# Optimization experiments

Hardware: AMD Instinct MI355X
Metric: run time of the kernel (lower is better)

## Reference

```python
import jax, jax.numpy as jnp
import numpy as np

H = 4          # heads
C = 32         # out_channels per head
NEG_SLOPE = 0.2
N_NODES = 50000
N_EDGES = 600000
F_IN = 128
OUT_DIM = 10
N_GRAPHS = 32


def _gat_params(keys, f_in, scale=0.05):
    hc = H * C
    return dict(
        Wl=jax.random.normal(keys[0], (f_in, hc)) * scale,
        bl=jnp.zeros((hc,)),
        Wr=jax.random.normal(keys[1], (f_in, hc)) * scale,
        br=jnp.zeros((hc,)),
        We=jax.random.normal(keys[2], (1, hc)) * scale,   # lin_edge, bias=False in PyG
        att=jax.random.normal(keys[3], (H, C)) * scale,
        bias=jnp.zeros((hc,)),
    )


def setup_inputs() -> dict:
    key = jax.random.key(0)
    ks = jax.random.split(key, 16)
    x = jax.random.normal(ks[0], (N_NODES, F_IN), dtype=jnp.float32)
    edge_index = jax.random.randint(ks[1], (2, N_EDGES), 0, N_NODES, dtype=jnp.int32)
    edge_weight = jax.random.uniform(ks[2], (N_EDGES, 1), dtype=jnp.float32)
    batch = jnp.sort(jax.random.randint(ks[3], (N_NODES,), 0, N_GRAPHS, dtype=jnp.int32))
    p1 = _gat_params(ks[4:8], F_IN)
    p2 = _gat_params(ks[8:12], H * C)
    fc_W = jax.random.normal(ks[12], (H * C, OUT_DIM)) * 0.05
    fc_b = jnp.zeros((OUT_DIM,))
    return dict(
        x=x, edge_index=edge_index, edge_weight=edge_weight, batch=batch,
        p1_Wl=p1['Wl'], p1_bl=p1['bl'], p1_Wr=p1['Wr'], p1_br=p1['br'],
        p1_We=p1['We'], p1_att=p1['att'], p1_bias=p1['bias'],
        p2_Wl=p2['Wl'], p2_bl=p2['bl'], p2_Wr=p2['Wr'], p2_br=p2['br'],
        p2_We=p2['We'], p2_att=p2['att'], p2_bias=p2['bias'],
        fc_W=fc_W, fc_b=fc_b,
    )


def _add_self_loops(src, dst, eattr, n):
    # PyG fill_value='mean': self-loop attr = mean of incoming edge_attr per node
    loop = jnp.arange(n, dtype=src.dtype)
    cnt = jax.ops.segment_sum(jnp.ones((src.shape[0],), eattr.dtype), dst, num_segments=n)
    loop_attr = jax.ops.segment_sum(eattr, dst, num_segments=n) / jnp.maximum(cnt, 1.0)[:, None]
    return (jnp.concatenate([src, loop]), jnp.concatenate([dst, loop]),
            jnp.concatenate([eattr, loop_attr], axis=0))


def _gatv2_conv(x, src, dst, eattr, Wl, bl, Wr, br, We, att, bias, n):
    x_l = (x @ Wl + bl).reshape(n, H, C)   # source transform
    x_r = (x @ Wr + br).reshape(n, H, C)   # target transform
    e_feat = (eattr @ We).reshape(-1, H, C)
    # per-edge message [E2, H, C]
    m = jax.nn.leaky_relu(x_l[src] + x_r[dst] + e_feat, NEG_SLOPE)
    alpha = jnp.einsum('ehc,hc->eh', m, att)            # [E2, H]
    amax = jax.ops.segment_max(alpha, dst, num_segments=n)
    amax = jnp.where(jnp.isfinite(amax), amax, 0.0)
    ex = jnp.exp(alpha - amax[dst])
    denom = jax.ops.segment_sum(ex, dst, num_segments=n)
    a = ex / (denom[dst] + 1e-16)                       # segment softmax
    out = jax.ops.segment_sum(a[:, :, None] * x_l[src], dst, num_segments=n)
    return out.reshape(n, H * C) + bias


def reference(x, edge_index, edge_weight, batch,
              p1_Wl, p1_bl, p1_Wr, p1_br, p1_We, p1_att, p1_bias,
              p2_Wl, p2_bl, p2_Wr, p2_br, p2_We, p2_att, p2_bias,
              fc_W, fc_b):
    n = x.shape[0]
    src, dst, eattr = _add_self_loops(edge_index[0], edge_index[1], edge_weight, n)
    h = _gatv2_conv(x, src, dst, eattr, p1_Wl, p1_bl, p1_Wr, p1_br, p1_We, p1_att, p1_bias, n)
    h = _gatv2_conv(h, src, dst, eattr, p2_Wl, p2_bl, p2_Wr, p2_br, p2_We, p2_att, p2_bias, n)
    cnt = jax.ops.segment_sum(jnp.ones((n,), h.dtype), batch, num_segments=N_GRAPHS)
    pooled = jax.ops.segment_sum(h, batch, num_segments=N_GRAPHS) / jnp.maximum(cnt, 1.0)[:, None]
    out = pooled @ fc_W + fc_b
    return out, pooled
```

## Files before the change

### kernel.cpp

```cpp
#include <hip/hip_runtime.h>
#include <hip/hip_bf16.h>
#include <cstdint>

static inline int cdiv(int a, int b){ return (a + b - 1) / b; }

typedef __attribute__((ext_vector_type(8))) short short8v;
typedef __attribute__((ext_vector_type(4))) float float4v;

#define ELLW 48

__device__ inline float bf2f(unsigned short u){ return __uint_as_float(((unsigned)u) << 16); }
__device__ inline unsigned short f2bf(float f){
  unsigned u = __float_as_uint(f);
  u += 0x7fffu + ((u >> 16) & 1u);
  return (unsigned short)(u >> 16);
}
__device__ inline float4 ldbf4(const unsigned short* p){
  ushort4 u = *(const ushort4*)p;
  return make_float4(bf2f(u.x), bf2f(u.y), bf2f(u.z), bf2f(u.w));
}
__device__ inline int sniff16(const unsigned* __restrict__ xw){
  int good = 0;
  #pragma unroll
  for (int j = 0; j < 16; ++j){
    float v = __uint_as_float(xw[j] << 16);
    float a = fabsf(v);
    good += (v == 0.f) || (a >= 6.1e-5f && a <= 64.f);
  }
  return good > 8;
}

struct P16 { const void* p[16]; };
__global__ void k_prep(P16 s, const unsigned* __restrict__ xw,
                       unsigned long long* __restrict__ deg64, float* __restrict__ pool,
                       int pz, int N,
                       unsigned short* __restrict__ Wf, unsigned short* __restrict__ bb,
                       unsigned short* __restrict__ sm){
  int i = blockIdx.x * blockDim.x + threadIdx.x;
  if (i < N) deg64[i] = 0ull;
  if (i < pz) pool[i] = 0.f;
  if (i >= 68106) return;
  const int bf = sniff16(xw);
  auto rd = [&](const void* q, int j) -> unsigned short {
    return bf ? ((const unsigned short*)q)[j] : f2bf(((const float*)q)[j]);
  };
  if (i < 65536){
    int l = i >> 15, r = i & 32767;
    int j = r & 7, n = (r >> 3) & 255, kq = r >> 11;
    int k = kq * 8 + j;
    const void* W = (n < 128) ? (l ? s.p[7] : s.p[0]) : (l ? s.p[9] : s.p[2]);
    Wf[i] = rd(W, k * 128 + (n & 127));
  } else if (i < 66048){
    int i2 = i - 65536;
    int l = i2 >> 8, n = i2 & 255;
    const void* b = (n < 128) ? (l ? s.p[8] : s.p[1]) : (l ? s.p[10] : s.p[3]);
    bb[i2] = rd(b, n & 127);
  } else {
    int j = i - 66048;
    const void* q; int o;
    if      (j < 128){ q = s.p[4];  o = j; }
    else if (j < 256){ q = s.p[5];  o = j - 128; }
    else if (j < 384){ q = s.p[6];  o = j - 256; }
    else if (j < 512){ q = s.p[11]; o = j - 384; }
    else if (j < 640){ q = s.p[12]; o = j - 512; }
    else if (j < 768){ q = s.p[13]; o = j - 640; }
    else if (j < 2048){ q = s.p[14]; o = j - 768; }
    else { q = s.p[15]; o = j - 2048; }
    sm[j] = rd(q, o);
  }
}

__global__ __launch_bounds__(256)
void k_esc(const int* __restrict__ ei, const void* __restrict__ ew,
           const unsigned* __restrict__ xw,
           unsigned long long* __restrict__ deg64, unsigned* __restrict__ eE,
           int E, int P, int N){
  const int bf = sniff16(xw);
  const int part = blockIdx.x & 7;
  const int lo = part * P;
  const int hi = min(lo + P, N);
  const int base = (int)(blockIdx.x >> 3) * 2048;
  const int end = min(base + 2048, E);
  for (int e = base + (int)threadIdx.x; e < end; e += 256){
    int dst = ei[E + e];
    if (dst < lo || dst >= hi) continue;
    int src = ei[e];
    unsigned short w16; float w;
    if (bf){ w16 = ((const unsigned short*)ew)[e]; w = bf2f(w16); }
    else   { w = ((const float*)ew)[e]; w16 = f2bf(w); }
    unsigned long long pk = (1ull << 40) + (unsigned long long)(unsigned)(w * 1048576.0f + 0.5f);
    unsigned long long old = atomicAdd(&deg64[dst], pk);
    int pos = min((int)(old >> 40), ELLW - 1);
    eE[dst * ELLW + pos] = (unsigned)src | ((unsigned)w16 << 16);
  }
}

template<bool ACT_BF_FIXED>
__global__ __launch_bounds__(256)
void k_gemm2(const void* __restrict__ actv, const unsigned* __restrict__ xw,
             const unsigned short* __restrict__ Wf, const unsigned short* __restrict__ bb,
             unsigned short* __restrict__ outL, unsigned short* __restrict__ outR, int nrows){
  __shared__ unsigned short As[64][136];
  const int abf = ACT_BF_FIXED ? 1 : sniff16(xw);
  const int t = threadIdx.x;
  const int row0 = blockIdx.x * 64;
  for (int c = t; c < 2048; c += 256){
    int row = c >> 5, col4 = (c & 31) * 4;
    int r = row0 + row;
    ushort4 v = make_ushort4(0, 0, 0, 0);
    if (r < nrows){
      if (abf) v = *(const ushort4*)((const unsigned short*)actv + (size_t)r * 128 + col4);
      else {
        float4 f = *(const float4*)((const float*)actv + (size_t)r * 128 + col4);
        v.x = f2bf(f.x); v.y = f2bf(f.y); v.z = f2bf(f.z); v.w = f2bf(f.w);
      }
    }
    *(ushort4*)&As[row][col4] = v;
  }
  __syncthreads();
  const int wv = t >> 6, lane = t & 63;
  const int l15 = lane & 15, q = lane >> 4;
  #pragma unroll
  for (int half = 0; half < 2; ++half){
    const int ntb = wv * 4 + half * 2;
    short8v bfr[2][4];
    #pragma unroll
    for (int nt = 0; nt < 2; ++nt){
      int n = (ntb + nt) * 16 + l15;
      #pragma unroll
      for (int ks = 0; ks < 4; ++ks)
        bfr[nt][ks] = *(const short8v*)(Wf + ((((ks * 4 + q) * 256 + n)) << 3));
    }
    float4v acc[4][2];
    #pragma unroll
    for (int mi = 0; mi < 4; ++mi)
      #pragma unroll
      for (int nt = 0; nt < 2; ++nt)
        acc[mi][nt] = (float4v){0.f, 0.f, 0.f, 0.f};
    #pragma unroll
    for (int mi = 0; mi < 4; ++mi){
      short8v afr[4];
      #pragma unroll
      for (int ks = 0; ks < 4; ++ks)
        afr[ks] = *(const short8v*)&As[mi * 16 + l15][ks * 32 + q * 8];
      #pragma unroll
      for (int nt = 0; nt < 2; ++nt)
        #pragma unroll
        for (int ks = 0; ks < 4; ++ks)
          acc[mi][nt] = __builtin_amdgcn_mfma_f32_16x16x32_bf16(afr[ks], bfr[nt][ks], acc[mi][nt], 0, 0, 0);
    }
    #pragma unroll
    for (int nt = 0; nt < 2; ++nt){
      int n = (ntb + nt) * 16 + l15;
      float bias = bf2f(bb[n]);
      unsigned short* outp = (n < 128) ? outL : outR;
      int nc = n & 127;
      #pragma unroll
      for (int mi = 0; mi < 4; ++mi)
        #pragma unroll
        for (int rr = 0; rr < 4; ++rr){
          int grow = row0 + mi * 16 + q * 4 + rr;
          if (grow < nrows) outp[(size_t)grow * 128 + nc] = f2bf(acc[mi][nt][rr] + bias);
        }
    }
  }
}

__global__ __launch_bounds__(256)
void k_node(const unsigned short* __restrict__ A, const unsigned short* __restrict__ B,
            const unsigned long long* __restrict__ deg64, const unsigned* __restrict__ eE,
            const unsigned short* __restrict__ We, const unsigned short* __restrict__ att,
            const unsigned short* __restrict__ bias, unsigned short* __restrict__ H, int N){
  int node = (blockIdx.x * 256 + threadIdx.x) >> 5;
  if (node >= N) return;
  int lane = threadIdx.x & 31;
  unsigned long long v64 = deg64[node];
  int d = (int)(v64 >> 40);
  float ws = (float)(v64 & 0xFFFFFFFFFFull) * (1.0f / 1048576.0f);
  float lw = ws / fmaxf((float)d, 1.0f);
  int dc = min(d, ELLW);
  const unsigned* eb = eE + (size_t)node * ELLW;
  float4 xr = ldbf4(B + (size_t)node * 128 + lane * 4);
  float4 we = ldbf4(We + lane * 4);
  float4 at = ldbf4(att + lane * 4);
  float4 at6 = make_float4(at.x * 0.6f, at.y * 0.6f, at.z * 0.6f, at.w * 0.6f);
  float4 at4 = make_float4(at.x * 0.4f, at.y * 0.4f, at.z * 0.4f, at.w * 0.4f);
  float4 xls = ldbf4(A + (size_t)node * 128 + lane * 4);
  float a, s;
  a = fmaf(lw, we.x, xls.x + xr.x); s = fmaf(at6.x, a, at4.x * fabsf(a));
  a = fmaf(lw, we.y, xls.y + xr.y); s = fmaf(at6.y, a, fmaf(at4.y, fabsf(a), s));
  a = fmaf(lw, we.z, xls.z + xr.z); s = fmaf(at6.z, a, fmaf(at4.z, fabsf(a), s));
  a = fmaf(lw, we.w, xls.w + xr.w); s = fmaf(at6.w, a, fmaf(at4.w, fabsf(a), s));
  s += __shfl_xor(s, 1);
  s += __shfl_xor(s, 2);
  s += __shfl_xor(s, 4);
  float exs = __expf(fminf(s, 60.f));
  float denom = exs;
  float4 acc = make_float4(exs * xls.x, exs * xls.y, exs * xls.z, exs * xls.w);
  int last = dc - 1;
  for (int p = 0; p < dc; p += 4){
    uint4 ev;
    if (p + 4 <= dc){
      ev = *(const uint4*)(eb + p);
    } else {
      ev.x = eb[p];
      ev.y = eb[min(p + 1, last)];
      ev.z = eb[min(p + 2, last)];
      ev.w = eb[min(p + 3, last)];
    }
    int i0 = ev.x & 0xffff, i1 = ev.y & 0xffff, i2 = ev.z & 0xffff, i3 = ev.w & 0xffff;
    float w0 = bf2f((unsigned short)(ev.x >> 16));
    float w1 = bf2f((unsigned short)(ev.y >> 16));
    float w2 = bf2f((unsigned short)(ev.z >> 16));
    float w3 = bf2f((unsigned short)(ev.w >> 16));
    float4 xl0 = ldbf4(A + (size_t)i0 * 128 + lane * 4);
    float4 xl1 = ldbf4(A + (size_t)i1 * 128 + lane * 4);
    float4 xl2 = ldbf4(A + (size_t)i2 * 128 + lane * 4);
    float4 xl3 = ldbf4(A + (size_t)i3 * 128 + lane * 4);
    float s0, s1, s2, s3;
    a = fmaf(w0, we.x, xl0.x + xr.x); s0 = fmaf(at6.x, a, at4.x * fabsf(a));
    a = fmaf(w0, we.y, xl0.y + xr.y); s0 = fmaf(at6.y, a, fmaf(at4.y, fabsf(a), s0));
    a = fmaf(w0, we.z, xl0.z + xr.z); s0 = fmaf(at6.z, a, fmaf(at4.z, fabsf(a), s0));
    a = fmaf(w0, we.w, xl0.w + xr.w); s0 = fmaf(at6.w, a, fmaf(at4.w, fabsf(a), s0));
    a = fmaf(w1, we.x, xl1.x + xr.x); s1 = fmaf(at6.x, a, at4.x * fabsf(a));
    a = fmaf(w1, we.y, xl1.y + xr.y); s1 = fmaf(at6.y, a, fmaf(at4.y, fabsf(a), s1));
    a = fmaf(w1, we.z, xl1.z + xr.z); s1 = fmaf(at6.z, a, fmaf(at4.z, fabsf(a), s1));
    a = fmaf(w1, we.w, xl1.w + xr.w); s1 = fmaf(at6.w, a, fmaf(at4.w, fabsf(a), s1));
    a = fmaf(w2, we.x, xl2.x + xr.x); s2 = fmaf(at6.x, a, at4.x * fabsf(a));
    a = fmaf(w2, we.y, xl2.y + xr.y); s2 = fmaf(at6.y, a, fmaf(at4.y, fabsf(a), s2));
    a = fmaf(w2, we.z, xl2.z + xr.z); s2 = fmaf(at6.z, a, fmaf(at4.z, fabsf(a), s2));
    a = fmaf(w2, we.w, xl2.w + xr.w); s2 = fmaf(at6.w, a, fmaf(at4.w, fabsf(a), s2));
    a = fmaf(w3, we.x, xl3.x + xr.x); s3 = fmaf(at6.x, a, at4.x * fabsf(a));
    a = fmaf(w3, we.y, xl3.y + xr.y); s3 = fmaf(at6.y, a, fmaf(at4.y, fabsf(a), s3));
    a = fmaf(w3, we.z, xl3.z + xr.z); s3 = fmaf(at6.z, a, fmaf(at4.z, fabsf(a), s3));
    a = fmaf(w3, we.w, xl3.w + xr.w); s3 = fmaf(at6.w, a, fmaf(at4.w, fabsf(a), s3));
    s0 += __shfl_xor(s0, 1); s1 += __shfl_xor(s1, 1); s2 += __shfl_xor(s2, 1); s3 += __shfl_xor(s3, 1);
    s0 += __shfl_xor(s0, 2); s1 += __shfl_xor(s1, 2); s2 += __shfl_xor(s2, 2); s3 += __shfl_xor(s3, 2);
    s0 += __shfl_xor(s0, 4); s1 += __shfl_xor(s1, 4); s2 += __shfl_xor(s2, 4); s3 += __shfl_xor(s3, 4);
    float ex0 = __expf(fminf(s0, 60.f));
    float ex1 = __expf(fminf(s1, 60.f));
    float ex2 = __expf(fminf(s2, 60.f));
    float ex3 = __expf(fminf(s3, 60.f));
    if (p + 1 >= dc) ex1 = 0.f;
    if (p + 2 >= dc) ex2 = 0.f;
    if (p + 3 >= dc) ex3 = 0.f;
    denom += (ex0 + ex1) + (ex2 + ex3);
    acc.x = fmaf(ex0, xl0.x, fmaf(ex1, xl1.x, fmaf(ex2, xl2.x, fmaf(ex3, xl3.x, acc.x))));
    acc.y = fmaf(ex0, xl0.y, fmaf(ex1, xl1.y, fmaf(ex2, xl2.y, fmaf(ex3, xl3.y, acc.y))));
    acc.z = fmaf(ex0, xl0.z, fmaf(ex1, xl1.z, fmaf(ex2, xl2.z, fmaf(ex3, xl3.z, acc.z))));
    acc.w = fmaf(ex0, xl0.w, fmaf(ex1, xl1.w, fmaf(ex2, xl2.w, fmaf(ex3, xl3.w, acc.w))));
  }
  float inv = 1.f / (denom + 1e-16f);
  float4 bv = ldbf4(bias + lane * 4);
  ushort4 o;
  o.x = f2bf(fmaf(acc.x, inv, bv.x));
  o.y = f2bf(fmaf(acc.y, inv, bv.y));
  o.z = f2bf(fmaf(acc.z, inv, bv.z));
  o.w = f2bf(fmaf(acc.w, inv, bv.w));
  *(ushort4*)(H + (size_t)node * 128 + lane * 4) = o;
}

__global__ __launch_bounds__(256)
void k_pool(const unsigned short* __restrict__ Cb, const int* __restrict__ batch,
            float* __restrict__ pool, float* __restrict__ gcnt, int N){
  __shared__ float sp[4][128];
  __shared__ float scnt[4];
  const int t = threadIdx.x;
  const int lane = t & 31, grp = t >> 5;
  const int r0 = blockIdx.x * 64;
  const int r1 = min(r0 + 64, N);
  if (r0 >= N) return;
  const int gmin = batch[r0];
  const int gmax = batch[r1 - 1];
  const int ngr = gmax - gmin + 1;
  const bool fits = (ngr <= 4);
  if (t < 4) scnt[t] = 0.f;
  for (int i = t; i < 4 * 128; i += 256) ((float*)sp)[i] = 0.f;
  __syncthreads();
  int curg = -1; float4 s = make_float4(0.f, 0.f, 0.f, 0.f); float cnt = 0.f;
  for (int r = r0 + grp; r < r1; r += 8){
    int g = batch[r];
    if (g != curg){
      if (curg >= 0){
        if (fits){
          float* pp = sp[curg - gmin] + lane * 4;
          atomicAdd(pp + 0, s.x); atomicAdd(pp + 1, s.y);
          atomicAdd(pp + 2, s.z); atomicAdd(pp + 3, s.w);
          if (lane == 0) atomicAdd(&scnt[curg - gmin], cnt);
        } else {
          float* pp = pool + (size_t)curg * 128 + lane * 4;
          atomicAdd(pp + 0, s.x); atomicAdd(pp + 1, s.y);
          atomicAdd(pp + 2, s.z); atomicAdd(pp + 3, s.w);
          if (lane == 0) atomicAdd(&gcnt[curg], cnt);
        }
      }
      s = make_float4(0.f, 0.f, 0.f, 0.f); cnt = 0.f; curg = g;
    }
    float4 v = ldbf4(Cb + (size_t)r * 128 + lane * 4);
    s.x += v.x; s.y += v.y; s.z += v.z; s.w += v.w;
    cnt += 1.f;
  }
  if (curg >= 0){
    if (fits){
      float* pp = sp[curg - gmin] + lane * 4;
      atomicAdd(pp + 0, s.x); atomicAdd(pp + 1, s.y);
      atomicAdd(pp + 2, s.z); atomicAdd(pp + 3, s.w);
      if (lane == 0) atomicAdd(&scnt[curg - gmin], cnt);
    } else {
      float* pp = pool + (size_t)curg * 128 + lane * 4;
      atomicAdd(pp + 0, s.x); atomicAdd(pp + 1, s.y);
      atomicAdd(pp + 2, s.z); atomicAdd(pp + 3, s.w);
      if (lane == 0) atomicAdd(&gcnt[curg], cnt);
    }
  }
  __syncthreads();
  if (fits){
    for (int i = t; i < ngr * 128; i += 256){
      int gg = i >> 7;
      atomicAdd(&pool[(size_t)(gmin + gg) * 128 + (i & 127)], ((float*)sp)[i]);
    }
    if (t < ngr) atomicAdd(&gcnt[gmin + t], scnt[t]);
  }
}

__global__ __launch_bounds__(256)
void k_fc(const float* __restrict__ pool, const float* __restrict__ gcnt,
          const unsigned short* __restrict__ fcW, const unsigned short* __restrict__ fcb,
          const unsigned* __restrict__ xw, void* __restrict__ outv, int G){
  __shared__ float sp[32 * 128];
  int t = threadIdx.x;
  int bf = sniff16(xw);
  unsigned short* ob = (unsigned short*)outv;
  float* of = (float*)outv;
  for (int idx = t; idx < G * 128; idx += 256){
    int g = idx >> 7;
    float p = pool[idx] / fmaxf(gcnt[g], 1.0f);
    sp[idx] = p;
    if (bf) ob[G * 10 + idx] = f2bf(p); else of[G * 10 + idx] = p;
  }
  __syncthreads();
  for (int idx = t; idx < G * 10; idx += 256){
    int g = idx / 10, o = idx - g * 10;
    float acc = bf2f(fcb[o]);
    const float* sg = sp + g * 128;
    #pragma unroll 4
    for (int c = 0; c < 128; ++c) acc = fmaf(sg[c], bf2f(fcW[c * 10 + o]), acc);
    if (bf) ob[idx] = f2bf(acc); else of[idx] = acc;
  }
}

extern "C" void kernel_launch(void* const* d_in, const int* in_sizes, int n_in,
                              void* d_out, int out_size, void* d_ws, size_t ws_size,
                              hipStream_t stream){
  const void* x    = d_in[0];
  const unsigned* xw = (const unsigned*)d_in[0];
  const int* ei    = (const int*)d_in[1];
  const void* ew   = d_in[2];
  const int* batch = (const int*)d_in[3];

  const int N  = in_sizes[3];
  const int E  = in_sizes[2];
  const int G  = out_size / 138;

  char* w = (char*)d_ws;
  auto take = [&](size_t nbytes) -> char* {
    char* p = w; w += (nbytes + 255) & ~(size_t)255; return p;
  };
  unsigned short* Abf  = (unsigned short*)take((size_t)N * 128 * 2);
  unsigned short* Bbf  = (unsigned short*)take((size_t)N * 128 * 2);
  unsigned short* Hb   = (unsigned short*)take((size_t)N * 128 * 2);
  unsigned long long* deg64 = (unsigned long long*)take((size_t)N * 8);
  unsigned* eE     = (unsigned*)take((size_t)N * ELLW * 4);
  float*    pool   = (float*)take((size_t)(G * 128 + G) * 4);
  float*    gcnt   = pool + (size_t)G * 128;
  unsigned short* Wf = (unsigned short*)take((size_t)2 * 32768 * 2);
  unsigned short* bb = (unsigned short*)take(512 * 2);
  unsigned short* sm = (unsigned short*)take(2058 * 2);

  P16 ps;
  for (int i = 0; i < 16; ++i) ps.p[i] = d_in[4 + i];
  const unsigned short* p1We = sm + 0;
  const unsigned short* p1at = sm + 128;
  const unsigned short* p1bs = sm + 256;
  const unsigned short* p2We = sm + 384;
  const unsigned short* p2at = sm + 512;
  const unsigned short* p2bs = sm + 640;
  const unsigned short* fcW  = sm + 768;
  const unsigned short* fcb  = sm + 2048;

  const int prepT = (68106 > N) ? 68106 : N;
  k_prep<<<cdiv(prepT, 256), 256, 0, stream>>>(ps, xw, deg64, pool, G * 128 + G, N, Wf, bb, sm);

  const int P = cdiv(N, 8);
  k_esc<<<cdiv(E, 2048) * 8, 256, 0, stream>>>(ei, ew, xw, deg64, eE, E, P, N);

  k_gemm2<false><<<cdiv(N, 64), 256, 0, stream>>>(x, xw, Wf, bb, Abf, Bbf, N);
  k_node<<<cdiv(N, 8), 256, 0, stream>>>(Abf, Bbf, deg64, eE, p1We, p1at, p1bs, Hb, N);

  k_gemm2<true><<<cdiv(N, 64), 256, 0, stream>>>(Hb, xw, Wf + 32768, bb + 256, Abf, Bbf, N);
  k_node<<<cdiv(N, 8), 256, 0, stream>>>(Abf, Bbf, deg64, eE, p2We, p2at, p2bs, Hb, N);

  k_pool<<<cdiv(N, 64), 256, 0, stream>>>(Hb, batch, pool, gcnt, N);
  k_fc<<<1, 256, 0, stream>>>(pool, gcnt, fcW, fcb, xw, d_out, G);
}
```

Measured before the change: 280.6 us.

## Stage GEMM epilogue through LDS for coalesced stores; fuse pool and FC via last-block ticket

The GEMM epilogue now writes bf16 results into a per-wave shared-memory tile and then stores 16-byte vectors per row, replacing scattered 2-byte global stores. The pooling and final FC kernels are merged into one launch: each block bumps an atomic counter after its pool atomics, and the last block to finish computes the mean and the FC output. This removes one kernel launch and its dependency gap, but adds a threadfence and an atomic ticket per block. The extra shared memory in the GEMM and in the fused kernel may lower occupancy.

```diff
diff --git a/kernel.cpp b/kernel.cpp
--- a/kernel.cpp
+++ b/kernel.cpp
@@ -33,12 +33,13 @@
 struct P16 { const void* p[16]; };
 __global__ void k_prep(P16 s, const unsigned* __restrict__ xw,
                        unsigned long long* __restrict__ deg64, float* __restrict__ pool,
-                       int pz, int N,
+                       unsigned* __restrict__ done, int pz, int N,
                        unsigned short* __restrict__ Wf, unsigned short* __restrict__ bb,
                        unsigned short* __restrict__ sm){
   int i = blockIdx.x * blockDim.x + threadIdx.x;
   if (i < N) deg64[i] = 0ull;
   if (i < pz) pool[i] = 0.f;
+  if (i == 0) done[0] = 0u;
   if (i >= 68106) return;
   const int bf = sniff16(xw);
   auto rd = [&](const void* q, int j) -> unsigned short {
@@ -101,6 +102,7 @@
              const unsigned short* __restrict__ Wf, const unsigned short* __restrict__ bb,
              unsigned short* __restrict__ outL, unsigned short* __restrict__ outR, int nrows){
   __shared__ unsigned short As[64][136];
+  __shared__ unsigned short Cs[4][64][40];
   const int abf = ACT_BF_FIXED ? 1 : sniff16(xw);
   const int t = threadIdx.x;
   const int row0 = blockIdx.x * 64;
@@ -153,15 +155,24 @@
     for (int nt = 0; nt < 2; ++nt){
       int n = (ntb + nt) * 16 + l15;
       float bias = bf2f(bb[n]);
-      unsigned short* outp = (n < 128) ? outL : outR;
-      int nc = n & 127;
       #pragma unroll
       for (int mi = 0; mi < 4; ++mi)
         #pragma unroll
-        for (int rr = 0; rr < 4; ++rr){
-          int grow = row0 + mi * 16 + q * 4 + rr;
-          if (grow < nrows) outp[(size_t)grow * 128 + nc] = f2bf(acc[mi][nt][rr] + bias);
-        }
+        for (int rr = 0; rr < 4; ++rr)
+          Cs[wv][mi * 16 + q * 4 + rr][nt * 16 + l15] = f2bf(acc[mi][nt][rr] + bias);
+    }
+    const int gb = wv * 64 + half * 32;
+    unsigned short* outp = (gb < 128) ? outL : outR;
+    const int gcol = gb & 127;
+    #pragma unroll
+    for (int k = 0; k < 4; ++k){
+      int q2 = lane + 64 * k;
+      int row = q2 >> 2, gc = q2 & 3;
+      int grow = row0 + row;
+      if (grow < nrows){
+        uint4 v = *(const uint4*)&Cs[wv][row][gc * 8];
+        *(uint4*)(outp + (size_t)grow * 128 + gcol + gc * 8) = v;
+      }
     }
   }
 }
@@ -261,15 +272,18 @@
 }
 
 __global__ __launch_bounds__(256)
-void k_pool(const unsigned short* __restrict__ Cb, const int* __restrict__ batch,
-            float* __restrict__ pool, float* __restrict__ gcnt, int N){
+void k_poolfc(const unsigned short* __restrict__ Cb, const int* __restrict__ batch,
+              float* __restrict__ pool, float* __restrict__ gcnt,
+              const unsigned short* __restrict__ fcW, const unsigned short* __restrict__ fcb,
+              const unsigned* __restrict__ xw, void* __restrict__ outv,
+              unsigned* __restrict__ done, int N, int G, int nblocks){
   __shared__ float sp[4][128];
   __shared__ float scnt[4];
+  __shared__ unsigned ticket;
   const int t = threadIdx.x;
   const int lane = t & 31, grp = t >> 5;
   const int r0 = blockIdx.x * 64;
   const int r1 = min(r0 + 64, N);
-  if (r0 >= N) return;
   const int gmin = batch[r0];
   const int gmax = batch[r1 - 1];
   const int ngr = gmax - gmin + 1;
@@ -321,28 +335,28 @@
     }
     if (t < ngr) atomicAdd(&gcnt[gmin + t], scnt[t]);
   }
-}
-
-__global__ __launch_bounds__(256)
-void k_fc(const float* __restrict__ pool, const float* __restrict__ gcnt,
-          const unsigned short* __restrict__ fcW, const unsigned short* __restrict__ fcb,
-          const unsigned* __restrict__ xw, void* __restrict__ outv, int G){
-  __shared__ float sp[32 * 128];
-  int t = threadIdx.x;
+  __threadfence();
+  __syncthreads();
+  if (t == 0) ticket = atomicAdd(done, 1u);
+  __syncthreads();
+  if (ticket != (unsigned)(nblocks - 1)) return;
+  __shared__ float sp2[32 * 128];
   int bf = sniff16(xw);
   unsigned short* ob = (unsigned short*)outv;
   float* of = (float*)outv;
   for (int idx = t; idx < G * 128; idx += 256){
     int g = idx >> 7;
-    float p = pool[idx] / fmaxf(gcnt[g], 1.0f);
-    sp[idx] = p;
+    float pv = atomicAdd(&pool[idx], 0.f);
+    float gc = atomicAdd(&gcnt[g], 0.f);
+    float p = pv / fmaxf(gc, 1.0f);
+    sp2[idx] = p;
     if (bf) ob[G * 10 + idx] = f2bf(p); else of[G * 10 + idx] = p;
   }
   __syncthreads();
   for (int idx = t; idx < G * 10; idx += 256){
     int g = idx / 10, o = idx - g * 10;
     float acc = bf2f(fcb[o]);
-    const float* sg = sp + g * 128;
+    const float* sg = sp2 + g * 128;
     #pragma unroll 4
     for (int c = 0; c < 128; ++c) acc = fmaf(sg[c], bf2f(fcW[c * 10 + o]), acc);
     if (bf) ob[idx] = f2bf(acc); else of[idx] = acc;
@@ -373,6 +387,7 @@
   unsigned* eE     = (unsigned*)take((size_t)N * ELLW * 4);
   float*    pool   = (float*)take((size_t)(G * 128 + G) * 4);
   float*    gcnt   = pool + (size_t)G * 128;
+  unsigned* done   = (unsigned*)take(4);
   unsigned short* Wf = (unsigned short*)take((size_t)2 * 32768 * 2);
   unsigned short* bb = (unsigned short*)take(512 * 2);
   unsigned short* sm = (unsigned short*)take(2058 * 2);
@@ -389,7 +404,7 @@
   const unsigned short* fcb  = sm + 2048;
 
   const int prepT = (68106 > N) ? 68106 : N;
-  k_prep<<<cdiv(prepT, 256), 256, 0, stream>>>(ps, xw, deg64, pool, G * 128 + G, N, Wf, bb, sm);
+  k_prep<<<cdiv(prepT, 256), 256, 0, stream>>>(ps, xw, deg64, pool, done, G * 128 + G, N, Wf, bb, sm);
 
   const int P = cdiv(N, 8);
   k_esc<<<cdiv(E, 2048) * 8, 256, 0, stream>>>(ei, ew, xw, deg64, eE, E, P, N);
@@ -400,6 +415,6 @@
   k_gemm2<true><<<cdiv(N, 64), 256, 0, stream>>>(Hb, xw, Wf + 32768, bb + 256, Abf, Bbf, N);
   k_node<<<cdiv(N, 8), 256, 0, stream>>>(Abf, Bbf, deg64, eE, p2We, p2at, p2bs, Hb, N);
 
-  k_pool<<<cdiv(N, 64), 256, 0, stream>>>(Hb, batch, pool, gcnt, N);
-  k_fc<<<1, 256, 0, stream>>>(pool, gcnt, fcW, fcb, xw, d_out, G);
-}
+  const int pb = cdiv(N, 64);
+  k_poolfc<<<pb, 256, 0, stream>>>(Hb, batch, pool, gcnt, fcW, fcb, xw, d_out, done, N, G, pb);
+}
```

Result: slower. 361.3 us (+28.8%).
